# Performance work log

Hardware: AMD Instinct MI355X
Metric: run time of the kernel (lower is better)

The kernel has to match this reference:

```python
import jax, jax.numpy as jnp
import numpy as np

B, S, E = 8, 2048, 256
NQ = 10
FF = 1024


def _cnot(state, c, t, n):
    # state: [T, 2^n]; wire 0 is the most-significant bit.
    T = state.shape[0]
    s = state.reshape((T,) + (2,) * n)
    ctrl0 = jnp.take(s, 0, axis=c + 1)
    ctrl1 = jnp.take(s, 1, axis=c + 1)
    # target axis index after removing the control axis
    t_ax = t + 1 if (t + 1) < (c + 1) else t
    ctrl1 = jnp.flip(ctrl1, axis=t_ax)  # X on target where control==1
    s = jnp.stack([ctrl0, ctrl1], axis=c + 1)
    return s.reshape(T, -1)


def _quantum_layer(tok, theta, n):
    # tok: [T, E] real; uses first n features as RX angles. Returns [T, n] PauliZ expvals.
    T = tok.shape[0]
    half = tok[:, :n] * 0.5
    c = jnp.cos(half).astype(jnp.complex64)
    s = (-1j * jnp.sin(half)).astype(jnp.complex64)
    # RX(theta)|0> = cos(t/2)|0> - i sin(t/2)|1>; build product state wire-by-wire
    state = jnp.ones((T, 1), dtype=jnp.complex64)
    for w in range(n):
        qb = jnp.stack([c[:, w], s[:, w]], axis=1)  # [T, 2]
        state = (state[:, :, None] * qb[:, None, :]).reshape(T, -1)
    # trainable RY per wire
    th = theta * 0.5
    for w in range(n):
        ct, st = jnp.cos(th[w]), jnp.sin(th[w])
        U = jnp.stack([jnp.stack([ct, -st]), jnp.stack([st, ct])]).astype(jnp.complex64)
        sr = state.reshape(T, 2 ** w, 2, -1)
        state = jnp.einsum('ij,tajb->taib', U, sr).reshape(T, -1)
    # CNOT ring
    for cw in range(n - 1):
        state = _cnot(state, cw, cw + 1, n)
    state = _cnot(state, n - 1, 0, n)
    probs = state.real ** 2 + state.imag ** 2  # [T, 2^n]
    idx = jnp.arange(2 ** n)
    bits = (idx[None, :] >> (n - 1 - jnp.arange(n)[:, None])) & 1  # [n, 2^n]
    z = (1.0 - 2.0 * bits).astype(probs.dtype)
    return probs @ z.T  # [T, n]


def setup_inputs() -> dict:
    key = jax.random.key(0)
    ks = jax.random.split(key, 6)
    return {
        'x': jax.random.normal(ks[0], (B, S, E), dtype=jnp.float32),
        'theta': jax.random.normal(ks[1], (NQ,), dtype=jnp.float32),
        'w1': jax.random.normal(ks[2], (FF, NQ), dtype=jnp.float32) * (1.0 / np.sqrt(NQ)),
        'b1': jax.random.normal(ks[3], (FF,), dtype=jnp.float32) * 0.02,
        'w2': jax.random.normal(ks[4], (E, FF), dtype=jnp.float32) * (1.0 / np.sqrt(FF)),
        'b2': jax.random.normal(ks[5], (E,), dtype=jnp.float32) * 0.02,
    }


def reference(x, theta, w1, b1, w2, b2):
    b, s, e = x.shape
    n = theta.shape[0]
    q = _quantum_layer(x.reshape(b * s, e), theta, n).reshape(b, s, n)
    # dropout is identity in eval mode
    h = jax.nn.relu(q @ w1.T + b1)
    return h @ w2.T + b2
```

## Files before the change

### kernel.cpp

```cpp
#include <hip/hip_runtime.h>
#include <math.h>

typedef __attribute__((ext_vector_type(8))) short bf16x8;
typedef __attribute__((ext_vector_type(4))) float f32x4;

#define T_TOT 16384
#define E_ 256
#define FF_ 1024
#define NQ 10
#define TB 64
#define CH 256
#define NCHUNK (FF_ / CH)
#define HGRAN (TB * CH)

__device__ __forceinline__ unsigned short f2bf(float f) {
    unsigned u = __builtin_bit_cast(unsigned, f);
    u = (u + 0x7FFFu + ((u >> 16) & 1u)) >> 16;
    return (unsigned short)u;
}

__global__ __launch_bounds__(256) void ffq_prep(
    const float* __restrict__ w2, const float* __restrict__ w1,
    uint4* __restrict__ w2f, uint4* __restrict__ w1f)
{
    int id = blockIdx.x * 256 + threadIdx.x;
    if (id < 32768) {
        int n  = id >> 7;
        int k0 = (id & 127) * 8;
        const float4* s = (const float4*)(w2 + (size_t)n * FF_ + k0);
        float4 a = s[0], b = s[1];
        uint4 v;
        v.x = f2bf(a.x) | ((unsigned)f2bf(a.y) << 16);
        v.y = f2bf(a.z) | ((unsigned)f2bf(a.w) << 16);
        v.z = f2bf(b.x) | ((unsigned)f2bf(b.y) << 16);
        v.w = f2bf(b.z) | ((unsigned)f2bf(b.w) << 16);
        int idx = ((k0 >> 5) * 16 + (n >> 4)) * 64 + ((k0 >> 3) & 3) * 16 + (n & 15);
        w2f[idx] = v;
    } else if (id < 32768 + 4096) {
        int id2 = id - 32768;
        int l = id2 & 63, nt = id2 >> 6;
        int n = nt * 16 + (l & 15);
        int g = l >> 4;
        unsigned short o[8];
#pragma unroll
        for (int j = 0; j < 8; ++j) {
            int k = g * 8 + j;
            o[j] = (k < NQ) ? f2bf(w1[n * NQ + k]) : (unsigned short)0;
        }
        uint4 v;
        v.x = o[0] | ((unsigned)o[1] << 16);
        v.y = o[2] | ((unsigned)o[3] << 16);
        v.z = o[4] | ((unsigned)o[5] << 16);
        v.w = o[6] | ((unsigned)o[7] << 16);
        w1f[id2] = v;
    }
}

__global__ __launch_bounds__(512, 4) void ffq_mfma(
    const float* __restrict__ x, const float* __restrict__ theta,
    const float* __restrict__ b1, const float* __restrict__ b2,
    const bf16x8* __restrict__ w1f, const bf16x8* __restrict__ w2f,
    float* __restrict__ out)
{
    __shared__ unsigned short q_s[4 * 64 * 8];
    __shared__ unsigned short hs[2 * HGRAN];

    const int tid  = threadIdx.x;
    const int l    = tid & 63;
    const int wv   = tid >> 6;
    const int lr   = l & 15;
    const int g    = l >> 4;
    const int chb  = blockIdx.x & 1;
    const int tb   = (blockIdx.x >> 1) * TB;
    const int ncol = chb * 8 + wv;

    if (tid < TB) {
        const int t = tb + tid;
        float xv[NQ];
        {
            float4 a = *(const float4*)(x + (size_t)t * E_);
            float4 b = *(const float4*)(x + (size_t)t * E_ + 4);
            float2 c = *(const float2*)(x + (size_t)t * E_ + 8);
            xv[0]=a.x; xv[1]=a.y; xv[2]=a.z; xv[3]=a.w;
            xv[4]=b.x; xv[5]=b.y; xv[6]=b.z; xv[7]=b.w;
            xv[8]=c.x; xv[9]=c.y;
        }
        float mm[NQ];
#pragma unroll
        for (int w = 0; w < NQ; ++w) mm[w] = cosf(theta[w]) * cosf(xv[w]);
        float qv[NQ];
        {
            float p = mm[0];
#pragma unroll
            for (int w = 1; w < NQ; ++w) { p *= mm[w]; qv[w] = p; }
            float p0 = mm[1];
#pragma unroll
            for (int w = 2; w < NQ; ++w) p0 *= mm[w];
            qv[0] = p0;
        }
        unsigned short qb[10];
#pragma unroll
        for (int k = 0; k < NQ; ++k) qb[k] = f2bf(qv[k]);
        uint4 s0, s1;
        s0.x = qb[0] | ((unsigned)qb[1] << 16);
        s0.y = qb[2] | ((unsigned)qb[3] << 16);
        s0.z = qb[4] | ((unsigned)qb[5] << 16);
        s0.w = qb[6] | ((unsigned)qb[7] << 16);
        s1.x = qb[8] | ((unsigned)qb[9] << 16);
        s1.y = 0; s1.z = 0; s1.w = 0;
        int tt = tid >> 4, r = tid & 15;
        uint4* base = (uint4*)q_s + tt * 64;
        base[r]      = s0;
        base[16 + r] = s1;
        base[32 + r] = make_uint4(0, 0, 0, 0);
        base[48 + r] = make_uint4(0, 0, 0, 0);
    }
    __syncthreads();

    bf16x8 qf[4];
#pragma unroll
    for (int tt = 0; tt < 4; ++tt) qf[tt] = ((const bf16x8*)q_s)[tt * 64 + l];

    f32x4 acc[4];
#pragma unroll
    for (int tt = 0; tt < 4; ++tt) acc[tt] = (f32x4){0.f, 0.f, 0.f, 0.f};

#define H_PHASE(cc, hdst, wfa)                                                 \
    {                                                                          \
        _Pragma("unroll")                                                      \
        for (int fi = 0; fi < 2; ++fi) {                                       \
            const int ftl = wv * 2 + fi;                                       \
            const int ntg = (cc) * 16 + ftl;                                   \
            const int f0  = ntg * 16 + g * 4;                                  \
            float4 bb = *(const float4*)(b1 + f0);                             \
            const int fl   = ftl * 16 + g * 4;                                 \
            const int sl   = (fl & 31) >> 3;                                   \
            const int gran = (fl >> 5) * 64 + lr + 16 * sl;                    \
            _Pragma("unroll")                                                  \
            for (int tt = 0; tt < 4; ++tt) {                                   \
                f32x4 d = {0.f, 0.f, 0.f, 0.f};                                \
                d = __builtin_amdgcn_mfma_f32_16x16x32_bf16(                   \
                        (wfa)[fi], qf[tt], d, 0, 0, 0);                        \
                unsigned p0 = f2bf(fmaxf(d[0] + bb.x, 0.f))                    \
                            | ((unsigned)f2bf(fmaxf(d[1] + bb.y, 0.f)) << 16); \
                unsigned p1 = f2bf(fmaxf(d[2] + bb.z, 0.f))                    \
                            | ((unsigned)f2bf(fmaxf(d[3] + bb.w, 0.f)) << 16); \
                unsigned byteoff = (unsigned)(tt * 512 + gran) * 16u           \
                                 + (unsigned)(fl & 7) * 2u;                    \
                *(uint2*)((char*)(hdst) + byteoff) = make_uint2(p0, p1);       \
            }                                                                  \
        }                                                                      \
    }

    {
        bf16x8 wf0[2];
        wf0[0] = w1f[(0 * 16 + wv * 2 + 0) * 64 + l];
        wf0[1] = w1f[(0 * 16 + wv * 2 + 1) * 64 + l];
        H_PHASE(0, hs, wf0)
    }
    bf16x8 bcur = w2f[(0 * 16 + ncol) * 64 + l];
    __syncthreads();

    for (int c = 0; c < NCHUNK; ++c) {
        const int cur = c & 1;
        const unsigned short* hcur = hs + cur * HGRAN;
        unsigned short*       hnxt = hs + (cur ^ 1) * HGRAN;

        const int cn = (c < NCHUNK - 1) ? c + 1 : NCHUNK - 1;
        bf16x8 wfn[2];
        wfn[0] = w1f[(cn * 16 + wv * 2 + 0) * 64 + l];
        wfn[1] = w1f[(cn * 16 + wv * 2 + 1) * 64 + l];

#pragma unroll
        for (int kkl = 0; kkl < 8; ++kkl) {
            const int kk  = c * 8 + kkl;
            const int kkn = (kk + 1 < 32) ? kk + 1 : 31;
            bf16x8 bnext = w2f[(kkn * 16 + ncol) * 64 + l];
            bf16x8 af[4];
#pragma unroll
            for (int tt = 0; tt < 4; ++tt)
                af[tt] = ((const bf16x8*)hcur)[(tt * 8 + kkl) * 64 + l];
#pragma unroll
            for (int tt = 0; tt < 4; ++tt)
                acc[tt] = __builtin_amdgcn_mfma_f32_16x16x32_bf16(
                    af[tt], bcur, acc[tt], 0, 0, 0);
            bcur = bnext;
        }

        if (c < NCHUNK - 1) {
            H_PHASE(c + 1, hnxt, wfn)
        }
        __syncthreads();
    }
#undef H_PHASE

    {
        const int col = ncol * 16 + lr;
        const float bbv = b2[col];
#pragma unroll
        for (int tt = 0; tt < 4; ++tt) {
#pragma unroll
            for (int r = 0; r < 4; ++r) {
                int tr = tb + tt * 16 + g * 4 + r;
                out[(size_t)tr * E_ + col] = acc[tt][r] + bbv;
            }
        }
    }
}

extern "C" void kernel_launch(void* const* d_in, const int* in_sizes, int n_in,
                              void* d_out, int out_size, void* d_ws, size_t ws_size,
                              hipStream_t stream) {
    const float* x     = (const float*)d_in[0];
    const float* theta = (const float*)d_in[1];
    const float* w1    = (const float*)d_in[2];
    const float* b1    = (const float*)d_in[3];
    const float* w2    = (const float*)d_in[4];
    const float* b2    = (const float*)d_in[5];
    float* out = (float*)d_out;

    uint4* w2f = (uint4*)d_ws;
    uint4* w1f = (uint4*)((char*)d_ws + 512 * 1024);

    hipLaunchKernelGGL(ffq_prep, dim3(144), dim3(256), 0, stream,
                       w2, w1, w2f, w1f);
    hipLaunchKernelGGL(ffq_mfma, dim3(2 * T_TOT / TB), dim3(512), 0, stream,
                       x, theta, b1, b2,
                       (const bf16x8*)w1f, (const bf16x8*)w2f, out);
}
```

Measured before the change: 27.06 us.

## Split second GEMM K across wave pairs with two column tiles per wave

Reassigns the eight waves so each handles two output column tiles over half of every K chunk, reusing each loaded h fragment for two MFMAs instead of one. Partial sums from the second wave group are reduced through shared memory before the bias add and store. The w1 fragment prefetch is replaced by an inline load inside the h phase. This halves LDS reads of h per MFMA but adds a cross-wave reduction, an extra barrier and more accumulator registers.

```diff
diff --git a/kernel.cpp b/kernel.cpp
--- a/kernel.cpp
+++ b/kernel.cpp
@@ -70,9 +70,12 @@
     const int wv   = tid >> 6;
     const int lr   = l & 15;
     const int g    = l >> 4;
+    const int wk   = wv >> 2;
+    const int wc   = wv & 3;
     const int chb  = blockIdx.x & 1;
     const int tb   = (blockIdx.x >> 1) * TB;
-    const int ncol = chb * 8 + wv;
+    const int nc0  = chb * 8 + wc * 2;
+    const int nc1  = nc0 + 1;
 
     if (tid < TB) {
         const int t = tb + tid;
@@ -121,16 +124,19 @@
 #pragma unroll
     for (int tt = 0; tt < 4; ++tt) qf[tt] = ((const bf16x8*)q_s)[tt * 64 + l];
 
-    f32x4 acc[4];
-#pragma unroll
-    for (int tt = 0; tt < 4; ++tt) acc[tt] = (f32x4){0.f, 0.f, 0.f, 0.f};
-
-#define H_PHASE(cc, hdst, wfa)                                                 \
+    f32x4 acc[4][2];
+#pragma unroll
+    for (int tt = 0; tt < 4; ++tt)
+#pragma unroll
+        for (int nn = 0; nn < 2; ++nn) acc[tt][nn] = (f32x4){0.f,0.f,0.f,0.f};
+
+#define H_PHASE(cc, hdst)                                                      \
     {                                                                          \
         _Pragma("unroll")                                                      \
         for (int fi = 0; fi < 2; ++fi) {                                       \
             const int ftl = wv * 2 + fi;                                       \
             const int ntg = (cc) * 16 + ftl;                                   \
+            bf16x8 wf = w1f[ntg * 64 + l];                                     \
             const int f0  = ntg * 16 + g * 4;                                  \
             float4 bb = *(const float4*)(b1 + f0);                             \
             const int fl   = ftl * 16 + g * 4;                                 \
@@ -140,7 +146,7 @@
             for (int tt = 0; tt < 4; ++tt) {                                   \
                 f32x4 d = {0.f, 0.f, 0.f, 0.f};                                \
                 d = __builtin_amdgcn_mfma_f32_16x16x32_bf16(                   \
-                        (wfa)[fi], qf[tt], d, 0, 0, 0);                        \
+                        wf, qf[tt], d, 0, 0, 0);                               \
                 unsigned p0 = f2bf(fmaxf(d[0] + bb.x, 0.f))                    \
                             | ((unsigned)f2bf(fmaxf(d[1] + bb.y, 0.f)) << 16); \
                 unsigned p1 = f2bf(fmaxf(d[2] + bb.z, 0.f))                    \
@@ -152,57 +158,77 @@
         }                                                                      \
     }
 
-    {
-        bf16x8 wf0[2];
-        wf0[0] = w1f[(0 * 16 + wv * 2 + 0) * 64 + l];
-        wf0[1] = w1f[(0 * 16 + wv * 2 + 1) * 64 + l];
-        H_PHASE(0, hs, wf0)
-    }
-    bf16x8 bcur = w2f[(0 * 16 + ncol) * 64 + l];
+    H_PHASE(0, hs)
+    bf16x8 bc0 = w2f[((wk * 4) * 16 + nc0) * 64 + l];
+    bf16x8 bc1 = w2f[((wk * 4) * 16 + nc1) * 64 + l];
     __syncthreads();
 
     for (int c = 0; c < NCHUNK; ++c) {
-        const int cur = c & 1;
-        const unsigned short* hcur = hs + cur * HGRAN;
-        unsigned short*       hnxt = hs + (cur ^ 1) * HGRAN;
-
-        const int cn = (c < NCHUNK - 1) ? c + 1 : NCHUNK - 1;
-        bf16x8 wfn[2];
-        wfn[0] = w1f[(cn * 16 + wv * 2 + 0) * 64 + l];
-        wfn[1] = w1f[(cn * 16 + wv * 2 + 1) * 64 + l];
-
-#pragma unroll
-        for (int kkl = 0; kkl < 8; ++kkl) {
+        const unsigned short* hcur = hs + (c & 1) * HGRAN;
+        unsigned short*       hnxt = hs + ((c & 1) ^ 1) * HGRAN;
+
+#pragma unroll
+        for (int j = 0; j < 4; ++j) {
+            const int kkl = wk * 4 + j;
             const int kk  = c * 8 + kkl;
-            const int kkn = (kk + 1 < 32) ? kk + 1 : 31;
-            bf16x8 bnext = w2f[(kkn * 16 + ncol) * 64 + l];
+            const int kkn = (j < 3) ? kk + 1
+                          : ((c < NCHUNK - 1) ? kk + 5 : kk);
+            bf16x8 bn0 = w2f[(kkn * 16 + nc0) * 64 + l];
+            bf16x8 bn1 = w2f[(kkn * 16 + nc1) * 64 + l];
             bf16x8 af[4];
 #pragma unroll
             for (int tt = 0; tt < 4; ++tt)
                 af[tt] = ((const bf16x8*)hcur)[(tt * 8 + kkl) * 64 + l];
 #pragma unroll
             for (int tt = 0; tt < 4; ++tt)
-                acc[tt] = __builtin_amdgcn_mfma_f32_16x16x32_bf16(
-                    af[tt], bcur, acc[tt], 0, 0, 0);
-            bcur = bnext;
+                acc[tt][0] = __builtin_amdgcn_mfma_f32_16x16x32_bf16(
+                    af[tt], bc0, acc[tt][0], 0, 0, 0);
+#pragma unroll
+            for (int tt = 0; tt < 4; ++tt)
+                acc[tt][1] = __builtin_amdgcn_mfma_f32_16x16x32_bf16(
+                    af[tt], bc1, acc[tt][1], 0, 0, 0);
+            bc0 = bn0; bc1 = bn1;
         }
 
         if (c < NCHUNK - 1) {
-            H_PHASE(c + 1, hnxt, wfn)
+            H_PHASE(c + 1, hnxt)
         }
         __syncthreads();
     }
 #undef H_PHASE
 
-    {
-        const int col = ncol * 16 + lr;
-        const float bbv = b2[col];
-#pragma unroll
-        for (int tt = 0; tt < 4; ++tt) {
-#pragma unroll
-            for (int r = 0; r < 4; ++r) {
-                int tr = tb + tt * 16 + g * 4 + r;
-                out[(size_t)tr * E_ + col] = acc[tt][r] + bbv;
+    float* pbuf = (float*)hs;
+    const int idx = wc * 64 + l;
+    if (wk == 1) {
+#pragma unroll
+        for (int tt = 0; tt < 4; ++tt)
+#pragma unroll
+            for (int nn = 0; nn < 2; ++nn)
+#pragma unroll
+                for (int r = 0; r < 4; ++r)
+                    pbuf[idx * 33 + (tt * 2 + nn) * 4 + r] = acc[tt][nn][r];
+    }
+    __syncthreads();
+    if (wk == 0) {
+#pragma unroll
+        for (int tt = 0; tt < 4; ++tt)
+#pragma unroll
+            for (int nn = 0; nn < 2; ++nn)
+#pragma unroll
+                for (int r = 0; r < 4; ++r)
+                    acc[tt][nn][r] += pbuf[idx * 33 + (tt * 2 + nn) * 4 + r];
+
+#pragma unroll
+        for (int nn = 0; nn < 2; ++nn) {
+            const int col = (nc0 + nn) * 16 + lr;
+            const float bbv = b2[col];
+#pragma unroll
+            for (int tt = 0; tt < 4; ++tt) {
+#pragma unroll
+                for (int r = 0; r < 4; ++r) {
+                    int tr = tb + tt * 16 + g * 4 + r;
+                    out[(size_t)tr * E_ + col] = acc[tt][nn][r] + bbv;
+                }
             }
         }
     }
```

Measured after the change: 27.20 us. No clear change (+0.5%).
